# Kernel optimization log

Hardware: AMD Instinct MI355X
Metric: run time of the kernel (lower is better)

## Reference

```python
import jax, jax.numpy as jnp
import numpy as np

N, C, H, W = 512, 512, 14, 14
CH, CW = 7, 7  # RoIAlign crop size


def conv1x1(x, w, b):
    # x: [N,C,H,W], w: [O,C], b: [O]  (1x1 conv == channel GEMM)
    return jnp.einsum('nchw,oc->nohw', x, w) + b[None, :, None, None]


def roi_align_fpcoor(x, boxes, ch, cw):
    """RoIAlign(transform_fpcoor=True) as in longcw/RoIAlign.pytorch.
    x: [N,C,H,W]; boxes: [N,4] = (x1,y1,x2,y2) in feature-pixel coords,
    box n crops image n. Returns [N,C,ch,cw]."""
    Hf, Wf = x.shape[2], x.shape[3]
    x1, y1, x2, y2 = boxes[:, 0], boxes[:, 1], boxes[:, 2], boxes[:, 3]
    sw = (x2 - x1) / cw
    sh = (y2 - y1) / ch
    nx0 = (x1 + sw * 0.5 - 0.5) / (Wf - 1)
    ny0 = (y1 + sh * 0.5 - 0.5) / (Hf - 1)
    nw = sw * (cw - 1) / (Wf - 1)
    nh = sh * (ch - 1) / (Hf - 1)
    # tf.crop_and_resize sample coordinates (crop size > 1 branch)
    ys = ny0[:, None] * (Hf - 1) + jnp.arange(ch, dtype=x.dtype) * (nh[:, None] * (Hf - 1) / (ch - 1))  # [N,ch]
    xs = nx0[:, None] * (Wf - 1) + jnp.arange(cw, dtype=x.dtype) * (nw[:, None] * (Wf - 1) / (cw - 1))  # [N,cw]
    y0f = jnp.floor(ys); x0f = jnp.floor(xs)
    wy = (ys - y0f)[:, :, None, None]          # [N,ch,1,1]
    wx = (xs - x0f)[:, None, :, None]          # [N,1,cw,1]
    y0 = jnp.clip(y0f.astype(jnp.int32), 0, Hf - 1)
    y1i = jnp.clip(y0 + 1, 0, Hf - 1)
    x0 = jnp.clip(x0f.astype(jnp.int32), 0, Wf - 1)
    x1i = jnp.clip(x0 + 1, 0, Wf - 1)
    b = jnp.arange(x.shape[0])[:, None, None]  # [N,1,1]
    yA = y0[:, :, None]; yB = y1i[:, :, None]  # [N,ch,1]
    xA = x0[:, None, :]; xB = x1i[:, None, :]  # [N,1,cw]
    # advanced indexing -> [N,ch,cw,C]
    v00 = x[b, :, yA, xA]; v01 = x[b, :, yA, xB]
    v10 = x[b, :, yB, xA]; v11 = x[b, :, yB, xB]
    top = v00 + (v01 - v00) * wx
    bot = v10 + (v11 - v10) * wx
    out = top + (bot - top) * wy               # [N,ch,cw,C]
    return jnp.transpose(out, (0, 3, 1, 2))    # [N,C,ch,cw]


def setup_inputs() -> dict:
    key = jax.random.key(0)
    ks = jax.random.split(key, 11)
    s = 0.02
    d = C * CH * CW  # 512*49
    return {
        'project': jax.random.normal(ks[0], (N, C, H, W), jnp.float32),
        'w1': jax.random.normal(ks[1], (C, C), jnp.float32) * s,
        'b1': jnp.zeros((C,), jnp.float32),
        'w2': jax.random.normal(ks[2], (C, C), jnp.float32) * s,
        'b2': jnp.zeros((C,), jnp.float32),
        'w3': jax.random.normal(ks[3], (C, C), jnp.float32) * s,
        'b3': jnp.zeros((C,), jnp.float32),
        'w_note': jax.random.normal(ks[4], (2, d), jnp.float32) * s,
        'b_note': jnp.zeros((2,), jnp.float32),
        'w_reg': jax.random.normal(ks[5], (8, d), jnp.float32) * s,
        'b_reg': jnp.zeros((8,), jnp.float32),
    }


def reference(project, w1, b1, w2, b2, w3, b3, w_note, b_note, w_reg, b_reg):
    x = conv1x1(project, w1, b1)
    x = conv1x1(x, w2, b2)
    # boxes are a fixed constant inside forward: [0,0,13,13] per RoI
    boxes = jnp.tile(jnp.asarray([[0.0, 0.0, 13.0, 13.0]], jnp.float32), (project.shape[0], 1))
    x = roi_align_fpcoor(x, boxes, CH, CW)     # [N,512,7,7]
    x = conv1x1(x, w3, b3)
    x = x.reshape((-1, C * CH * CW))
    note = x @ w_note.T + b_note
    reg = x @ w_reg.T + b_reg
    return note, reg
```

## Files before the change

kernel.cpp:

```cpp
#include <hip/hip_runtime.h>


#define CHW4 25088
#define STEP 1.8571428571428572f

__global__ __launch_bounds__(512) void k_prep1(
    const float* __restrict__ w_note, const float* __restrict__ w_reg,
    const float* __restrict__ w2, const float* __restrict__ b1,
    const float* __restrict__ b2,
    float* __restrict__ WH, float* __restrict__ u2) {
    int blk = blockIdx.x;
    int tid = threadIdx.x;
    if (blk < 490) {
        int k = blk / 49, ji = blk % 49;
        const float* wh = (k < 2) ? (w_note + k * 25088) : (w_reg + (k - 2) * 25088);
        WH[(size_t)blk * 512 + tid] = wh[tid * 49 + ji];
    } else {
        int wv = tid >> 6, lane = tid & 63;
        int o = (blk - 490) * 8 + wv;
        float s = 0.f;
        #pragma unroll
        for (int r = 0; r < 8; ++r) s += w2[(size_t)o * 512 + lane + r * 64] * b1[lane + r * 64];
        for (int off = 32; off; off >>= 1) s += __shfl_down(s, off);
        if (lane == 0) u2[o] = b2[o] + s;
    }
}

__global__ __launch_bounds__(256) void k_prep2(
    const float* __restrict__ w1, const float* __restrict__ w2,
    const float* __restrict__ w3, const float* __restrict__ WH,
    const float* __restrict__ u2, const float* __restrict__ b3,
    float* __restrict__ Y, float* __restrict__ T1, float* __restrict__ vv) {
    int blk = blockIdx.x;
    int tid = threadIdx.x;
    if (blk < 512) {
        __shared__ float As[32][36];
        __shared__ float Bs[32][36];
        const float* A; const float* B; float* C; int M;
        if (blk < 256) { A = w2; B = w1; C = Y;  M = 512; }
        else           { A = WH; B = w3; C = T1; M = 490; }
        int t = blk & 255;
        int bx = t & 15, by = t >> 4;
        int lr = tid >> 3, lc = (tid & 7) << 2;
        int tx = tid & 15, ty = tid >> 4;
        float a00 = 0.f, a01 = 0.f, a10 = 0.f, a11 = 0.f;
        for (int kc = 0; kc < 512; kc += 32) {
            int gr = by * 32 + lr;
            float4 av = make_float4(0.f, 0.f, 0.f, 0.f);
            if (gr < M) av = *(const float4*)&A[(size_t)gr * 512 + kc + lc];
            *(float4*)&As[lr][lc] = av;
            *(float4*)&Bs[lr][lc] = *(const float4*)&B[(size_t)(kc + lr) * 512 + bx * 32 + lc];
            __syncthreads();
            #pragma unroll
            for (int kk = 0; kk < 32; ++kk) {
                float b0 = Bs[kk][tx * 2], b1v = Bs[kk][tx * 2 + 1];
                float x0 = As[ty * 2][kk], x1 = As[ty * 2 + 1][kk];
                a00 += x0 * b0; a01 += x0 * b1v;
                a10 += x1 * b0; a11 += x1 * b1v;
            }
            __syncthreads();
        }
        int r0 = by * 32 + ty * 2, c0 = bx * 32 + tx * 2;
        if (r0 < M)     { C[(size_t)r0 * 512 + c0] = a00; C[(size_t)r0 * 512 + c0 + 1] = a01; }
        if (r0 + 1 < M) { C[(size_t)(r0 + 1) * 512 + c0] = a10; C[(size_t)(r0 + 1) * 512 + c0 + 1] = a11; }
    } else {
        int wv = tid >> 6, lane = tid & 63;
        int o = (blk - 512) * 4 + wv;
        float s = 0.f;
        #pragma unroll
        for (int r = 0; r < 8; ++r) s += w3[(size_t)o * 512 + lane + r * 64] * u2[lane + r * 64];
        for (int off = 32; off; off >>= 1) s += __shfl_down(s, off);
        if (lane == 0) vv[o] = b3[o] + s;
    }
}

__global__ __launch_bounds__(256) void k_prep3(
    const float* __restrict__ T1, const float* __restrict__ Y,
    const float* __restrict__ w_note, const float* __restrict__ w_reg,
    const float* __restrict__ vv,
    float* __restrict__ Bmat, float* __restrict__ dpart) {
    int blk = blockIdx.x;
    int tid = threadIdx.x;
    if (blk < 256) {
        __shared__ float As[32][36];
        __shared__ float Bs[32][36];
        int bx = blk & 15, by = blk >> 4;
        int lr = tid >> 3, lc = (tid & 7) << 2;
        int tx = tid & 15, ty = tid >> 4;
        int gr = by * 32 + lr;
        float a00 = 0.f, a01 = 0.f, a10 = 0.f, a11 = 0.f;
        for (int kc = 0; kc < 512; kc += 32) {
            float4 av = make_float4(0.f, 0.f, 0.f, 0.f);
            if (gr < 490) av = *(const float4*)&T1[(size_t)gr * 512 + kc + lc];
            *(float4*)&As[lr][lc] = av;
            *(float4*)&Bs[lr][lc] = *(const float4*)&Y[(size_t)(kc + lr) * 512 + bx * 32 + lc];
            __syncthreads();
            #pragma unroll
            for (int kk = 0; kk < 32; ++kk) {
                float b0 = Bs[kk][tx * 2], b1v = Bs[kk][tx * 2 + 1];
                float x0 = As[ty * 2][kk], x1 = As[ty * 2 + 1][kk];
                a00 += x0 * b0; a01 += x0 * b1v;
                a10 += x1 * b0; a11 += x1 * b1v;
            }
            __syncthreads();
        }
        int r0 = by * 32 + ty * 2, c0 = bx * 32 + tx * 2;
        if (r0 < 490)     { Bmat[(size_t)r0 * 512 + c0] = a00; Bmat[(size_t)r0 * 512 + c0 + 1] = a01; }
        if (r0 + 1 < 490) { Bmat[(size_t)(r0 + 1) * 512 + c0] = a10; Bmat[(size_t)(r0 + 1) * 512 + c0 + 1] = a11; }
    } else {
        int t = blk - 256;
        int k = t >> 3, b8 = t & 7;
        const float* wh = (k < 2) ? (w_note + k * 25088) : (w_reg + (k - 2) * 25088);
        float s = 0.f;
        for (int i = b8 * 256 + tid; i < 25088; i += 2048) s += wh[i] * vv[i / 49];
        __shared__ float red[256];
        red[tid] = s;
        __syncthreads();
        for (int off = 128; off; off >>= 1) {
            if (tid < off) red[tid] += red[tid + off];
            __syncthreads();
        }
        if (tid == 0) dpart[k * 8 + b8] = red[0];
    }
}

__global__ __launch_bounds__(256) void k_mainf(const float* __restrict__ proj,
                                               const float* __restrict__ Bmat,
                                               float* __restrict__ part) {
    __shared__ float X[2][16][197];
    int b = blockIdx.x;
    int n = b >> 1;
    int ch0 = (b & 1) << 4;
    int tid = threadIdx.x;
    int wv = tid >> 6, lane = tid & 63;

    int cc0 = tid / 49,            q0 = tid - cc0 * 49;
    int cc1 = cc0 + 5,             q1 = q0 + 11; if (q1 >= 49) { q1 -= 49; ++cc1; }
    int cc2 = cc1 + 5,             q2 = q1 + 11; if (q2 >= 49) { q2 -= 49; ++cc2; }

    const float base = STEP * 0.5f - 0.5f;
    int   i00s[4], bidx0s[4];
    float wxs[4], wys[4];
    #pragma unroll
    for (int s = 0; s < 4; ++s) {
        int o = tid + s * 256;
        if (o > 783) o = 783;
        int ji = o >> 4, cl = o & 15;
        int j = (ji * 37) >> 8;
        int i2 = ji - j * 7;
        float yv = base + j * STEP;
        float xv = base + i2 * STEP;
        float y0f = floorf(yv), x0f = floorf(xv);
        wys[s] = yv - y0f; wxs[s] = xv - x0f;
        i00s[s] = cl * 197 + (int)y0f * 14 + (int)x0f;
        bidx0s[s] = (ji << 9) + cl;
    }

    const float4* src0 = (const float4*)proj + (size_t)n * CHW4 + ch0 * 784;
    float acc[10];
    #pragma unroll
    for (int k = 0; k < 10; ++k) acc[k] = 0.f;

    {
        float4 v0 = src0[tid];
        float4 v1 = src0[tid + 256];
        float4 v2 = src0[tid + 512];
        float* xb = &X[0][0][0];
        *(float4*)&xb[cc0 * 197 + q0 * 4] = v0;
        *(float4*)&xb[cc1 * 197 + q1 * 4] = v1;
        *(float4*)&xb[cc2 * 197 + q2 * 4] = v2;
        if (tid < 16) *(float4*)&xb[15 * 197 + (tid + 33) * 4] = src0[tid + 768];
    }
    __syncthreads();

    int cur = 0;
    #pragma unroll 1
    for (int t = 0; t < 16; ++t) {
        float4 v0, v1, v2, v3;
        if (t < 15) {
            const float4* sn = src0 + (t + 1) * 784;
            v0 = sn[tid]; v1 = sn[tid + 256]; v2 = sn[tid + 512];
            if (tid < 16) v3 = sn[tid + 768];
        }
        const float* xb = &X[cur][0][0];
        int ch = ch0 + t;
        const float* Bc = Bmat + (ch << 4);
        #pragma unroll
        for (int s = 0; s < 3; ++s) {
            int i00 = i00s[s];
            float v00 = xb[i00],      v01 = xb[i00 + 1];
            float v10 = xb[i00 + 14], v11 = xb[i00 + 15];
            float top = v00 + (v01 - v00) * wxs[s];
            float bot = v10 + (v11 - v10) * wxs[s];
            float v = top + (bot - top) * wys[s];
            const float* Bp = Bc + bidx0s[s];
            #pragma unroll
            for (int k = 0; k < 10; ++k)
                acc[k] += v * Bp[(size_t)k * 25088];
        }
        if (tid < 16) {
            int i00 = i00s[3];
            float v00 = xb[i00],      v01 = xb[i00 + 1];
            float v10 = xb[i00 + 14], v11 = xb[i00 + 15];
            float top = v00 + (v01 - v00) * wxs[3];
            float bot = v10 + (v11 - v10) * wxs[3];
            float v = top + (bot - top) * wys[3];
            const float* Bp = Bc + bidx0s[3];
            #pragma unroll
            for (int k = 0; k < 10; ++k)
                acc[k] += v * Bp[(size_t)k * 25088];
        }
        if (t < 15) {
            float* xw = &X[cur ^ 1][0][0];
            *(float4*)&xw[cc0 * 197 + q0 * 4] = v0;
            *(float4*)&xw[cc1 * 197 + q1 * 4] = v1;
            *(float4*)&xw[cc2 * 197 + q2 * 4] = v2;
            if (tid < 16) *(float4*)&xw[15 * 197 + (tid + 33) * 4] = v3;
        }
        __syncthreads();
        cur ^= 1;
    }

    #pragma unroll
    for (int k = 0; k < 10; ++k) {
        float v = acc[k];
        v += __shfl_xor(v, 1);
        v += __shfl_xor(v, 2);
        v += __shfl_xor(v, 4);
        v += __shfl_xor(v, 8);
        v += __shfl_xor(v, 16);
        v += __shfl_xor(v, 32);
        if (lane == k) part[((size_t)b * 4 + wv) * 10 + k] = v;
    }
}

__global__ void k_reduce(const float* __restrict__ part,
                         const float* __restrict__ dpart,
                         const float* __restrict__ b_note, const float* __restrict__ b_reg,
                         float* __restrict__ out) {
    int idx = blockIdx.x * 256 + threadIdx.x;
    int n = idx / 10, k = idx % 10;
    float s = (k < 2) ? b_note[k] : b_reg[k - 2];
    for (int b = 0; b < 8; ++b) s += dpart[k * 8 + b];
    #pragma unroll
    for (int h = 0; h < 2; ++h)
        for (int w = 0; w < 4; ++w)
            s += part[(((size_t)(n * 2 + h)) * 4 + w) * 10 + k];
    if (k < 2) out[n * 2 + k] = s;
    else       out[1024 + n * 8 + (k - 2)] = s;
}

extern "C" void kernel_launch(void* const* d_in, const int* in_sizes, int n_in,
                              void* d_out, int out_size, void* d_ws, size_t ws_size,
                              hipStream_t stream) {
    const float* proj   = (const float*)d_in[0];
    const float* w1     = (const float*)d_in[1];
    const float* b1     = (const float*)d_in[2];
    const float* w2     = (const float*)d_in[3];
    const float* b2     = (const float*)d_in[4];
    const float* w3     = (const float*)d_in[5];
    const float* b3     = (const float*)d_in[6];
    const float* w_note = (const float*)d_in[7];
    const float* b_note = (const float*)d_in[8];
    const float* w_reg  = (const float*)d_in[9];
    const float* b_reg  = (const float*)d_in[10];

    float* ws    = (float*)d_ws;
    float* WH    = ws;
    float* Y     = WH + 250880;
    float* T1    = Y + 262144;
    float* Bmat  = T1 + 250880;
    float* u2    = Bmat + 250880;
    float* vv    = u2 + 512;
    float* dpart = vv + 512;
    float* part  = dpart + 80;
    float* out   = (float*)d_out;

    k_prep1<<<554, 512, 0, stream>>>(w_note, w_reg, w2, b1, b2, WH, u2);
    k_prep2<<<640, 256, 0, stream>>>(w1, w2, w3, WH, u2, b3, Y, T1, vv);
    k_prep3<<<336, 256, 0, stream>>>(T1, Y, w_note, w_reg, vv, Bmat, dpart);
    k_mainf<<<1024, 256, 0, stream>>>(proj, Bmat, part);
    k_reduce<<<20, 256, 0, stream>>>(part, dpart, b_note, b_reg, out);
}
```

Measured before the change: 95.37 us.

## Swap main-kernel work split so fused weights stay in registers across images

Each block of the main kernel now owns one 16-channel group across 16 images, instead of one image across 16 channel groups. The fused projection coefficients are loaded into registers once per thread rather than re-read from global memory on every iteration. The input staging becomes a two-deep register prefetch pipeline with a custom LDS barrier. In exchange, per-block partial sums now go to a much larger buffer (128 partials per image), so the reduce kernel does more work and the workspace must be larger.

```diff
diff --git a/kernel.cpp b/kernel.cpp
--- a/kernel.cpp
+++ b/kernel.cpp
@@ -3,6 +3,13 @@
 
 #define CHW4 25088
 #define STEP 1.8571428571428572f
+
+#define BAR() do { \
+    __builtin_amdgcn_sched_barrier(0); \
+    asm volatile("s_waitcnt lgkmcnt(0)" ::: "memory"); \
+    __builtin_amdgcn_s_barrier(); \
+    __builtin_amdgcn_sched_barrier(0); \
+} while (0)
 
 __global__ __launch_bounds__(512) void k_prep1(
     const float* __restrict__ w_note, const float* __restrict__ w_reg,
@@ -129,22 +136,22 @@
                                                float* __restrict__ part) {
     __shared__ float X[2][16][197];
     int b = blockIdx.x;
-    int n = b >> 1;
-    int ch0 = (b & 1) << 4;
+    int g = b & 31;
+    int n0 = (b >> 5) << 4;
     int tid = threadIdx.x;
     int wv = tid >> 6, lane = tid & 63;
 
-    int cc0 = tid / 49,            q0 = tid - cc0 * 49;
-    int cc1 = cc0 + 5,             q1 = q0 + 11; if (q1 >= 49) { q1 -= 49; ++cc1; }
-    int cc2 = cc1 + 5,             q2 = q1 + 11; if (q2 >= 49) { q2 -= 49; ++cc2; }
+    int cc0 = tid / 49, q0 = tid - cc0 * 49;
+    int cc1 = cc0 + 5, q1 = q0 + 11; if (q1 >= 49) { q1 -= 49; ++cc1; }
+    int cc2 = cc1 + 5, q2 = q1 + 11; if (q2 >= 49) { q2 -= 49; ++cc2; }
 
     const float base = STEP * 0.5f - 0.5f;
-    int   i00s[4], bidx0s[4];
+    int i00s[4];
     float wxs[4], wys[4];
+    float Bm[4][10];
     #pragma unroll
     for (int s = 0; s < 4; ++s) {
-        int o = tid + s * 256;
-        if (o > 783) o = 783;
+        int o = tid + s * 256; if (o > 783) o = 783;
         int ji = o >> 4, cl = o & 15;
         int j = (ji * 37) >> 8;
         int i2 = ji - j * 7;
@@ -153,85 +160,84 @@
         float y0f = floorf(yv), x0f = floorf(xv);
         wys[s] = yv - y0f; wxs[s] = xv - x0f;
         i00s[s] = cl * 197 + (int)y0f * 14 + (int)x0f;
-        bidx0s[s] = (ji << 9) + cl;
-    }
-
-    const float4* src0 = (const float4*)proj + (size_t)n * CHW4 + ch0 * 784;
-    float acc[10];
-    #pragma unroll
-    for (int k = 0; k < 10; ++k) acc[k] = 0.f;
-
-    {
-        float4 v0 = src0[tid];
-        float4 v1 = src0[tid + 256];
-        float4 v2 = src0[tid + 512];
-        float* xb = &X[0][0][0];
-        *(float4*)&xb[cc0 * 197 + q0 * 4] = v0;
-        *(float4*)&xb[cc1 * 197 + q1 * 4] = v1;
-        *(float4*)&xb[cc2 * 197 + q2 * 4] = v2;
-        if (tid < 16) *(float4*)&xb[15 * 197 + (tid + 33) * 4] = src0[tid + 768];
-    }
-    __syncthreads();
-
-    int cur = 0;
+        int bidx = (ji << 9) + (g << 4) + cl;
+        #pragma unroll
+        for (int k = 0; k < 10; ++k) Bm[s][k] = Bmat[(size_t)k * 25088 + bidx];
+    }
+
+    const float4* src = (const float4*)proj + (size_t)n0 * CHW4 + g * 784;
+
+#define ISSUE(T, R0, R1, R2, R3) do { \
+    const float4* sn_ = src + (size_t)(T) * CHW4; \
+    R0 = sn_[tid]; R1 = sn_[tid + 256]; R2 = sn_[tid + 512]; \
+    if (tid < 16) R3 = sn_[tid + 768]; \
+} while (0)
+
+#define SCATTER(BUF, R0, R1, R2, R3) do { \
+    float* xw_ = &X[BUF][0][0]; \
+    *(float4*)&xw_[cc0 * 197 + q0 * 4] = R0; \
+    *(float4*)&xw_[cc1 * 197 + q1 * 4] = R1; \
+    *(float4*)&xw_[cc2 * 197 + q2 * 4] = R2; \
+    if (tid < 16) *(float4*)&xw_[15 * 197 + (tid + 33) * 4] = R3; \
+} while (0)
+
+#define COMPUTE_STORE(T, BUF) do { \
+    const float* xb_ = &X[BUF][0][0]; \
+    float acc[10]; \
+    _Pragma("unroll") for (int k = 0; k < 10; ++k) acc[k] = 0.f; \
+    _Pragma("unroll") for (int s = 0; s < 3; ++s) { \
+        int i00 = i00s[s]; \
+        float v00 = xb_[i00],      v01 = xb_[i00 + 1]; \
+        float v10 = xb_[i00 + 14], v11 = xb_[i00 + 15]; \
+        float top = v00 + (v01 - v00) * wxs[s]; \
+        float bot = v10 + (v11 - v10) * wxs[s]; \
+        float v = top + (bot - top) * wys[s]; \
+        _Pragma("unroll") for (int k = 0; k < 10; ++k) acc[k] += v * Bm[s][k]; \
+    } \
+    if (tid < 16) { \
+        int i00 = i00s[3]; \
+        float v00 = xb_[i00],      v01 = xb_[i00 + 1]; \
+        float v10 = xb_[i00 + 14], v11 = xb_[i00 + 15]; \
+        float top = v00 + (v01 - v00) * wxs[3]; \
+        float bot = v10 + (v11 - v10) * wxs[3]; \
+        float v = top + (bot - top) * wys[3]; \
+        _Pragma("unroll") for (int k = 0; k < 10; ++k) acc[k] += v * Bm[3][k]; \
+    } \
+    _Pragma("unroll") for (int k = 0; k < 10; ++k) { \
+        float v = acc[k]; \
+        v += __shfl_xor(v, 1);  v += __shfl_xor(v, 2);  v += __shfl_xor(v, 4); \
+        v += __shfl_xor(v, 8);  v += __shfl_xor(v, 16); v += __shfl_xor(v, 32); \
+        if (lane == k) \
+            part[(((size_t)(n0 + (T)) * 32 + g) * 4 + wv) * 10 + k] = v; \
+    } \
+} while (0)
+
+    float4 A0, A1, A2, A3, B0, B1, B2, B3;
+    ISSUE(0, A0, A1, A2, A3);
+    ISSUE(1, B0, B1, B2, B3);
+    SCATTER(0, A0, A1, A2, A3);
+    BAR();
+
     #pragma unroll 1
-    for (int t = 0; t < 16; ++t) {
-        float4 v0, v1, v2, v3;
-        if (t < 15) {
-            const float4* sn = src0 + (t + 1) * 784;
-            v0 = sn[tid]; v1 = sn[tid + 256]; v2 = sn[tid + 512];
-            if (tid < 16) v3 = sn[tid + 768];
-        }
-        const float* xb = &X[cur][0][0];
-        int ch = ch0 + t;
-        const float* Bc = Bmat + (ch << 4);
-        #pragma unroll
-        for (int s = 0; s < 3; ++s) {
-            int i00 = i00s[s];
-            float v00 = xb[i00],      v01 = xb[i00 + 1];
-            float v10 = xb[i00 + 14], v11 = xb[i00 + 15];
-            float top = v00 + (v01 - v00) * wxs[s];
-            float bot = v10 + (v11 - v10) * wxs[s];
-            float v = top + (bot - top) * wys[s];
-            const float* Bp = Bc + bidx0s[s];
-            #pragma unroll
-            for (int k = 0; k < 10; ++k)
-                acc[k] += v * Bp[(size_t)k * 25088];
-        }
-        if (tid < 16) {
-            int i00 = i00s[3];
-            float v00 = xb[i00],      v01 = xb[i00 + 1];
-            float v10 = xb[i00 + 14], v11 = xb[i00 + 15];
-            float top = v00 + (v01 - v00) * wxs[3];
-            float bot = v10 + (v11 - v10) * wxs[3];
-            float v = top + (bot - top) * wys[3];
-            const float* Bp = Bc + bidx0s[3];
-            #pragma unroll
-            for (int k = 0; k < 10; ++k)
-                acc[k] += v * Bp[(size_t)k * 25088];
-        }
-        if (t < 15) {
-            float* xw = &X[cur ^ 1][0][0];
-            *(float4*)&xw[cc0 * 197 + q0 * 4] = v0;
-            *(float4*)&xw[cc1 * 197 + q1 * 4] = v1;
-            *(float4*)&xw[cc2 * 197 + q2 * 4] = v2;
-            if (tid < 16) *(float4*)&xw[15 * 197 + (tid + 33) * 4] = v3;
-        }
-        __syncthreads();
-        cur ^= 1;
-    }
-
-    #pragma unroll
-    for (int k = 0; k < 10; ++k) {
-        float v = acc[k];
-        v += __shfl_xor(v, 1);
-        v += __shfl_xor(v, 2);
-        v += __shfl_xor(v, 4);
-        v += __shfl_xor(v, 8);
-        v += __shfl_xor(v, 16);
-        v += __shfl_xor(v, 32);
-        if (lane == k) part[((size_t)b * 4 + wv) * 10 + k] = v;
-    }
+    for (int tt = 0; tt < 7; ++tt) {
+        int t0 = tt * 2;
+        ISSUE(t0 + 2, A0, A1, A2, A3);
+        SCATTER(1, B0, B1, B2, B3);
+        COMPUTE_STORE(t0, 0);
+        BAR();
+        ISSUE(t0 + 3, B0, B1, B2, B3);
+        SCATTER(0, A0, A1, A2, A3);
+        COMPUTE_STORE(t0 + 1, 1);
+        BAR();
+    }
+    SCATTER(1, B0, B1, B2, B3);
+    COMPUTE_STORE(14, 0);
+    BAR();
+    COMPUTE_STORE(15, 1);
+
+#undef ISSUE
+#undef SCATTER
+#undef COMPUTE_STORE
 }
 
 __global__ void k_reduce(const float* __restrict__ part,
@@ -242,10 +248,7 @@
     int n = idx / 10, k = idx % 10;
     float s = (k < 2) ? b_note[k] : b_reg[k - 2];
     for (int b = 0; b < 8; ++b) s += dpart[k * 8 + b];
-    #pragma unroll
-    for (int h = 0; h < 2; ++h)
-        for (int w = 0; w < 4; ++w)
-            s += part[(((size_t)(n * 2 + h)) * 4 + w) * 10 + k];
+    for (int w = 0; w < 128; ++w) s += part[((size_t)n * 128 + w) * 10 + k];
     if (k < 2) out[n * 2 + k] = s;
     else       out[1024 + n * 8 + (k - 2)] = s;
 }
```

New measurement: 126.6 us. +32.8%, slower.

## Process four images per block in k_mainf to reuse Bmat coefficients

Applied to the files above, without the earlier changes.

The main kernel now assigns each block four images and a quarter of the channel range instead of one image and half the channels. Each thread loads its ten Bmat coefficients once per channel step and applies them to four images' bilinear samples, so Bmat traffic per image drops by roughly four. Loads are grouped with scheduling barriers to overlap the next tile's prefetch. In exchange it uses more registers (40 accumulators plus extra prefetch registers), launches half as many blocks, and writes a larger partial-sum array, and the reduction kernel is updated to match.

```diff
diff --git a/kernel.cpp b/kernel.cpp
--- a/kernel.cpp
+++ b/kernel.cpp
@@ -127,111 +127,146 @@
 __global__ __launch_bounds__(256) void k_mainf(const float* __restrict__ proj,
                                                const float* __restrict__ Bmat,
                                                float* __restrict__ part) {
-    __shared__ float X[2][16][197];
+    __shared__ float X[4][2][8][197];
     int b = blockIdx.x;
-    int n = b >> 1;
-    int ch0 = (b & 1) << 4;
+    int quad = b >> 2;
+    int qt = b & 3;
     int tid = threadIdx.x;
     int wv = tid >> 6, lane = tid & 63;
-
-    int cc0 = tid / 49,            q0 = tid - cc0 * 49;
-    int cc1 = cc0 + 5,             q1 = q0 + 11; if (q1 >= 49) { q1 -= 49; ++cc1; }
-    int cc2 = cc1 + 5,             q2 = q1 + 11; if (q2 >= 49) { q2 -= 49; ++cc2; }
+    int n0 = quad * 4;
+
+    int ldsOff[7], srcOff[7];
+    #pragma unroll
+    for (int s = 0; s < 7; ++s) {
+        int i = (s < 6) ? (tid + s * 256) : (1536 + tid);
+        if (i > 1567) i = 1567;
+        int row = i / 392, rem = i - row * 392;
+        int cc = rem / 49, q = rem - cc * 49;
+        ldsOff[s] = row * 3152 + cc * 197 + q * 4;
+        srcOff[s] = row * CHW4 + rem;
+    }
+    const float4* srcQ = (const float4*)proj + (size_t)n0 * CHW4 + qt * 6272;
 
     const float base = STEP * 0.5f - 0.5f;
-    int   i00s[4], bidx0s[4];
-    float wxs[4], wys[4];
+    int i00A, bidxA, i00B, bidxB;
+    float wxA, wyA, wxB, wyB;
+    {
+        int o = tid;
+        int ji = o >> 3, cl = o & 7;
+        int j = (ji * 37) >> 8, i2 = ji - j * 7;
+        float yv = base + j * STEP, xv = base + i2 * STEP;
+        float y0f = floorf(yv), x0f = floorf(xv);
+        wyA = yv - y0f; wxA = xv - x0f;
+        i00A = cl * 197 + (int)y0f * 14 + (int)x0f;
+        bidxA = ji * 512 + qt * 128 + cl;
+    }
+    {
+        int o = tid + 256; if (o > 391) o = 391;
+        int ji = o >> 3, cl = o & 7;
+        int j = (ji * 37) >> 8, i2 = ji - j * 7;
+        float yv = base + j * STEP, xv = base + i2 * STEP;
+        float y0f = floorf(yv), x0f = floorf(xv);
+        wyB = yv - y0f; wxB = xv - x0f;
+        i00B = cl * 197 + (int)y0f * 14 + (int)x0f;
+        bidxB = ji * 512 + qt * 128 + cl;
+    }
+    bool tB = tid < 136;
+    bool t32 = tid < 32;
+
+    float acc[4][10];
     #pragma unroll
-    for (int s = 0; s < 4; ++s) {
-        int o = tid + s * 256;
-        if (o > 783) o = 783;
-        int ji = o >> 4, cl = o & 15;
-        int j = (ji * 37) >> 8;
-        int i2 = ji - j * 7;
-        float yv = base + j * STEP;
-        float xv = base + i2 * STEP;
-        float y0f = floorf(yv), x0f = floorf(xv);
-        wys[s] = yv - y0f; wxs[s] = xv - x0f;
-        i00s[s] = cl * 197 + (int)y0f * 14 + (int)x0f;
-        bidx0s[s] = (ji << 9) + cl;
-    }
-
-    const float4* src0 = (const float4*)proj + (size_t)n * CHW4 + ch0 * 784;
-    float acc[10];
-    #pragma unroll
-    for (int k = 0; k < 10; ++k) acc[k] = 0.f;
-
-    {
-        float4 v0 = src0[tid];
-        float4 v1 = src0[tid + 256];
-        float4 v2 = src0[tid + 512];
-        float* xb = &X[0][0][0];
-        *(float4*)&xb[cc0 * 197 + q0 * 4] = v0;
-        *(float4*)&xb[cc1 * 197 + q1 * 4] = v1;
-        *(float4*)&xb[cc2 * 197 + q2 * 4] = v2;
-        if (tid < 16) *(float4*)&xb[15 * 197 + (tid + 33) * 4] = src0[tid + 768];
-    }
+    for (int r = 0; r < 4; ++r)
+        #pragma unroll
+        for (int k = 0; k < 10; ++k) acc[r][k] = 0.f;
+
+    float* xflat = &X[0][0][0][0];
+    float4 p0, p1, p2, p3, p4, p5, p6;
+
+    p0 = srcQ[srcOff[0]]; p1 = srcQ[srcOff[1]]; p2 = srcQ[srcOff[2]];
+    p3 = srcQ[srcOff[3]]; p4 = srcQ[srcOff[4]]; p5 = srcQ[srcOff[5]];
+    if (t32) p6 = srcQ[srcOff[6]];
+    *(float4*)&xflat[ldsOff[0]] = p0;
+    *(float4*)&xflat[ldsOff[1]] = p1;
+    *(float4*)&xflat[ldsOff[2]] = p2;
+    *(float4*)&xflat[ldsOff[3]] = p3;
+    *(float4*)&xflat[ldsOff[4]] = p4;
+    *(float4*)&xflat[ldsOff[5]] = p5;
+    if (t32) *(float4*)&xflat[ldsOff[6]] = p6;
     __syncthreads();
 
     int cur = 0;
     #pragma unroll 1
     for (int t = 0; t < 16; ++t) {
-        float4 v0, v1, v2, v3;
+        float cA[10], cB[10];
+        {
+            const float* BpA = Bmat + bidxA + t * 8;
+            #pragma unroll
+            for (int k = 0; k < 10; ++k) cA[k] = BpA[(size_t)k * 25088];
+            if (tB) {
+                const float* BpB = Bmat + bidxB + t * 8;
+                #pragma unroll
+                for (int k = 0; k < 10; ++k) cB[k] = BpB[(size_t)k * 25088];
+            }
+        }
+        __builtin_amdgcn_sched_barrier(0);
         if (t < 15) {
-            const float4* sn = src0 + (t + 1) * 784;
-            v0 = sn[tid]; v1 = sn[tid + 256]; v2 = sn[tid + 512];
-            if (tid < 16) v3 = sn[tid + 768];
-        }
-        const float* xb = &X[cur][0][0];
-        int ch = ch0 + t;
-        const float* Bc = Bmat + (ch << 4);
-        #pragma unroll
-        for (int s = 0; s < 3; ++s) {
-            int i00 = i00s[s];
-            float v00 = xb[i00],      v01 = xb[i00 + 1];
-            float v10 = xb[i00 + 14], v11 = xb[i00 + 15];
-            float top = v00 + (v01 - v00) * wxs[s];
-            float bot = v10 + (v11 - v10) * wxs[s];
-            float v = top + (bot - top) * wys[s];
-            const float* Bp = Bc + bidx0s[s];
-            #pragma unroll
-            for (int k = 0; k < 10; ++k)
-                acc[k] += v * Bp[(size_t)k * 25088];
-        }
-        if (tid < 16) {
-            int i00 = i00s[3];
-            float v00 = xb[i00],      v01 = xb[i00 + 1];
-            float v10 = xb[i00 + 14], v11 = xb[i00 + 15];
-            float top = v00 + (v01 - v00) * wxs[3];
-            float bot = v10 + (v11 - v10) * wxs[3];
-            float v = top + (bot - top) * wys[3];
-            const float* Bp = Bc + bidx0s[3];
-            #pragma unroll
-            for (int k = 0; k < 10; ++k)
-                acc[k] += v * Bp[(size_t)k * 25088];
+            const float4* sq = srcQ + (t + 1) * 392;
+            p0 = sq[srcOff[0]]; p1 = sq[srcOff[1]]; p2 = sq[srcOff[2]];
+            p3 = sq[srcOff[3]]; p4 = sq[srcOff[4]]; p5 = sq[srcOff[5]];
+            if (t32) p6 = sq[srcOff[6]];
+        }
+        __builtin_amdgcn_sched_barrier(0);
+        const float* xc = xflat + cur * 1576;
+        #pragma unroll
+        for (int r = 0; r < 4; ++r) {
+            const float* xr = xc + r * 3152 + i00A;
+            float v00 = xr[0], v01 = xr[1], v10 = xr[14], v11 = xr[15];
+            float top = v00 + (v01 - v00) * wxA;
+            float bot = v10 + (v11 - v10) * wxA;
+            float v = top + (bot - top) * wyA;
+            #pragma unroll
+            for (int k = 0; k < 10; ++k) acc[r][k] += v * cA[k];
+        }
+        if (tB) {
+            #pragma unroll
+            for (int r = 0; r < 4; ++r) {
+                const float* xr = xc + r * 3152 + i00B;
+                float v00 = xr[0], v01 = xr[1], v10 = xr[14], v11 = xr[15];
+                float top = v00 + (v01 - v00) * wxB;
+                float bot = v10 + (v11 - v10) * wxB;
+                float v = top + (bot - top) * wyB;
+                #pragma unroll
+                for (int k = 0; k < 10; ++k) acc[r][k] += v * cB[k];
+            }
         }
         if (t < 15) {
-            float* xw = &X[cur ^ 1][0][0];
-            *(float4*)&xw[cc0 * 197 + q0 * 4] = v0;
-            *(float4*)&xw[cc1 * 197 + q1 * 4] = v1;
-            *(float4*)&xw[cc2 * 197 + q2 * 4] = v2;
-            if (tid < 16) *(float4*)&xw[15 * 197 + (tid + 33) * 4] = v3;
+            float* xw = xflat + (cur ^ 1) * 1576;
+            *(float4*)&xw[ldsOff[0]] = p0;
+            *(float4*)&xw[ldsOff[1]] = p1;
+            *(float4*)&xw[ldsOff[2]] = p2;
+            *(float4*)&xw[ldsOff[3]] = p3;
+            *(float4*)&xw[ldsOff[4]] = p4;
+            *(float4*)&xw[ldsOff[5]] = p5;
+            if (t32) *(float4*)&xw[ldsOff[6]] = p6;
         }
         __syncthreads();
         cur ^= 1;
     }
 
     #pragma unroll
-    for (int k = 0; k < 10; ++k) {
-        float v = acc[k];
-        v += __shfl_xor(v, 1);
-        v += __shfl_xor(v, 2);
-        v += __shfl_xor(v, 4);
-        v += __shfl_xor(v, 8);
-        v += __shfl_xor(v, 16);
-        v += __shfl_xor(v, 32);
-        if (lane == k) part[((size_t)b * 4 + wv) * 10 + k] = v;
-    }
+    for (int r = 0; r < 4; ++r)
+        #pragma unroll
+        for (int k = 0; k < 10; ++k) {
+            float v = acc[r][k];
+            v += __shfl_xor(v, 1);
+            v += __shfl_xor(v, 2);
+            v += __shfl_xor(v, 4);
+            v += __shfl_xor(v, 8);
+            v += __shfl_xor(v, 16);
+            v += __shfl_xor(v, 32);
+            if (lane == r * 10 + k)
+                part[(((size_t)b * 4 + wv) * 4 + r) * 10 + k] = v;
+        }
 }
 
 __global__ void k_reduce(const float* __restrict__ part,
@@ -240,12 +275,13 @@
                          float* __restrict__ out) {
     int idx = blockIdx.x * 256 + threadIdx.x;
     int n = idx / 10, k = idx % 10;
+    int quad = n >> 2, r = n & 3;
     float s = (k < 2) ? b_note[k] : b_reg[k - 2];
-    for (int b = 0; b < 8; ++b) s += dpart[k * 8 + b];
+    for (int b8 = 0; b8 < 8; ++b8) s += dpart[k * 8 + b8];
     #pragma unroll
-    for (int h = 0; h < 2; ++h)
+    for (int qt = 0; qt < 4; ++qt)
         for (int w = 0; w < 4; ++w)
-            s += part[(((size_t)(n * 2 + h)) * 4 + w) * 10 + k];
+            s += part[((((size_t)(quad * 4 + qt)) * 4 + w) * 4 + r) * 10 + k];
     if (k < 2) out[n * 2 + k] = s;
     else       out[1024 + n * 8 + (k - 2)] = s;
 }
@@ -279,6 +315,6 @@
     k_prep1<<<554, 512, 0, stream>>>(w_note, w_reg, w2, b1, b2, WH, u2);
     k_prep2<<<640, 256, 0, stream>>>(w1, w2, w3, WH, u2, b3, Y, T1, vv);
     k_prep3<<<336, 256, 0, stream>>>(T1, Y, w_note, w_reg, vv, Bmat, dpart);
-    k_mainf<<<1024, 256, 0, stream>>>(proj, Bmat, part);
+    k_mainf<<<512, 256, 0, stream>>>(proj, Bmat, part);
     k_reduce<<<20, 256, 0, stream>>>(part, dpart, b_note, b_reg, out);
 }
```

After: 85.11 us. 10.8% less time.
